# Performance work log

Measured on AMD Instinct MI355X. Metric: run time of the kernel, lower is better.

## Reference

```python
import jax, jax.numpy as jnp
import numpy as np

IN_F, OUT_F = 4096, 4096
IN_Q, OUT_Q = IN_F // 4, OUT_F // 4


def setup_inputs() -> dict:
    key = jax.random.key(0)
    kx, kr, ki, kj, kk = jax.random.split(key, 5)
    std = 1.0 / np.sqrt(IN_F)
    x = jax.random.normal(kx, (4, 2048, IN_F), dtype=jnp.float32)
    Wr = std * jax.random.normal(kr, (OUT_Q, IN_Q), dtype=jnp.float32)
    Wi = std * jax.random.normal(ki, (OUT_Q, IN_Q), dtype=jnp.float32)
    Wj = std * jax.random.normal(kj, (OUT_Q, IN_Q), dtype=jnp.float32)
    Wk = std * jax.random.normal(kk, (OUT_Q, IN_Q), dtype=jnp.float32)
    bias = jnp.zeros((OUT_F,), dtype=jnp.float32)
    return {"x": x, "Wr": Wr, "Wi": Wi, "Wj": Wj, "Wk": Wk, "bias": bias}


def _hamilton_block(Wr, Wi, Wj, Wk):
    # Assemble the structured [4*out_q, 4*in_q] Hamilton block weight so the
    # whole op is ONE large GEMM instead of 16 small ones (same math).
    row_r = jnp.concatenate([Wr, -Wi, -Wj, -Wk], axis=1)
    row_i = jnp.concatenate([Wi,  Wr,  Wk, -Wj], axis=1)
    row_j = jnp.concatenate([Wj, -Wk,  Wr,  Wi], axis=1)
    row_k = jnp.concatenate([Wk,  Wj, -Wi,  Wr], axis=1)
    return jnp.concatenate([row_r, row_i, row_j, row_k], axis=0)  # [OUT_F, IN_F]


def reference(x, Wr, Wi, Wj, Wk, bias):
    W = _hamilton_block(Wr, Wi, Wj, Wk)
    # x: [B, S, IN_F] @ W.T -> [B, S, OUT_F]
    out = jnp.einsum('bsf,of->bso', x, W) + bias
    return out
```

## Files before the change

kernel.cpp:

```cpp
#include <hip/hip_runtime.h>
#include <hip/hip_bf16.h>


#define M_DIM 8192
#define N_DIM 4096
#define K_DIM 4096
#define BK 64
#define NT (K_DIM / BK)

typedef __attribute__((ext_vector_type(8))) short bf16x8;
typedef __attribute__((ext_vector_type(4))) float f32x4;
typedef __attribute__((ext_vector_type(8))) unsigned short ushort8;

static __device__ __forceinline__ unsigned short f2bf(float f) {
    unsigned int u = __float_as_uint(f);
    return (unsigned short)((u + 0x7fffu + ((u >> 16) & 1u)) >> 16);
}
static __device__ __forceinline__ unsigned short f2bf_sgn(float f, unsigned int sg) {
    unsigned int u = __float_as_uint(f) ^ sg;
    return (unsigned short)((u + 0x7fffu + ((u >> 16) & 1u)) >> 16);
}

__global__ __launch_bounds__(256) void cvt_x_kernel(const float* __restrict__ x,
                                                    unsigned short* __restrict__ xb) {
    int i = (blockIdx.x * 256 + threadIdx.x) * 8;
    f32x4 a = __builtin_nontemporal_load((const f32x4*)(x + i));
    f32x4 b = __builtin_nontemporal_load((const f32x4*)(x + i + 4));
    ushort8 o;
    o[0] = f2bf(a[0]); o[1] = f2bf(a[1]); o[2] = f2bf(a[2]); o[3] = f2bf(a[3]);
    o[4] = f2bf(b[0]); o[5] = f2bf(b[1]); o[6] = f2bf(b[2]); o[7] = f2bf(b[3]);
    *(ushort8*)(xb + i) = o;
}

__global__ __launch_bounds__(256) void prep_w_kernel(const float* __restrict__ Wr,
    const float* __restrict__ Wi, const float* __restrict__ Wj,
    const float* __restrict__ Wk, unsigned short* __restrict__ wb) {
    int row = blockIdx.x >> 1;
    int col = ((blockIdx.x & 1) * 256 + threadIdx.x) * 8;
    int p = row >> 10, q = col >> 10;
    int ci = p ^ q;
    const float* src = (ci == 0) ? Wr : (ci == 1) ? Wi : (ci == 2) ? Wj : Wk;
    unsigned int sg = ((0x428Eu >> (p * 4 + q)) & 1u) << 31;
    int so = (row & 1023) * 1024 + (col & 1023);
    f32x4 a = *(const f32x4*)(src + so);
    f32x4 b = *(const f32x4*)(src + so + 4);
    ushort8 o;
    o[0] = f2bf_sgn(a[0], sg); o[1] = f2bf_sgn(a[1], sg);
    o[2] = f2bf_sgn(a[2], sg); o[3] = f2bf_sgn(a[3], sg);
    o[4] = f2bf_sgn(b[0], sg); o[5] = f2bf_sgn(b[1], sg);
    o[6] = f2bf_sgn(b[2], sg); o[7] = f2bf_sgn(b[3], sg);
    *(ushort8*)(wb + row * 4096 + col) = o;
}

#define GLD16(gp, lp) __builtin_amdgcn_global_load_lds( \
    (const __attribute__((address_space(1))) void*)(gp), \
    (__attribute__((address_space(3))) void*)(lp), 16, 0, 0)

#define BAR() do { asm volatile("" ::: "memory"); \
                   __builtin_amdgcn_s_barrier(); \
                   asm volatile("" ::: "memory"); } while (0)
#define VM(n) asm volatile("s_waitcnt vmcnt(" #n ")" ::: "memory")

static __device__ __forceinline__ f32x4 MF(bf16x8 a, bf16x8 b, f32x4 c) {
    return __builtin_amdgcn_mfma_f32_16x16x32_bf16(a, b, c, 0, 0, 0);
}

__global__ __launch_bounds__(512, 2) void qgemm_bf16(
    const unsigned short* __restrict__ A, const unsigned short* __restrict__ B,
    const float* __restrict__ bias, float* __restrict__ out)
{
    __shared__ __align__(16) unsigned short Lsh[2][2][2][128 * 64];

    int bid = blockIdx.x;
    int cpx = gridDim.x >> 3;
    int wg  = (bid & 7) * cpx + (bid >> 3);
    int brow = (wg >> 4) * 256;
    int bcol = (wg & 15) * 256;

    int tid   = threadIdx.x;
    int lane  = tid & 63;
    int wid   = tid >> 6;
    int hA    = wid >> 2;
    int nb    = wid & 3;
    int hB    = nb >> 1;
    int rB0   = (nb & 1) << 6;
    int fr    = lane & 15;
    int fslot = lane >> 4;

    const unsigned short* Ag = A + (size_t)brow * K_DIM;
    const unsigned short* Bg = B + (size_t)bcol * K_DIM;

    f32x4 acc[8][4] = {};

    auto stage = [&](int buf, int ab, int half, int t) {
        const unsigned short* g = (ab ? Bg : Ag) + (size_t)(half << 7) * K_DIM + t * BK;
        unsigned short* l = &Lsh[buf][ab][half][0];
        #pragma unroll
        for (int i = 0; i < 2; ++i) {
            int c = i * 512 + tid;
            int r = c >> 3, s = c & 7;
            GLD16(g + (size_t)r * K_DIM + ((s ^ (r & 7)) << 3), l + (c << 3));
        }
    };
    auto rdA = [&](int buf, int mi, int ks) -> bf16x8 {
        int r = mi * 16 + fr;
        int slot = (ks * 4 + fslot) ^ (r & 7);
        return *(const bf16x8*)((const char*)&Lsh[buf][0][hA][0] + r * 128 + (slot << 4));
    };
    auto rdB = [&](int buf, int ni, int ks) -> bf16x8 {
        int r = rB0 + ni * 16 + fr;
        int slot = (ks * 4 + fslot) ^ (r & 7);
        return *(const bf16x8*)((const char*)&Lsh[buf][1][hB][0] + r * 128 + (slot << 4));
    };

    stage(0, 0, 0, 0); stage(0, 0, 1, 0); stage(0, 1, 0, 0); stage(0, 1, 1, 0);
    stage(1, 1, 0, 1); stage(1, 1, 1, 1);
    VM(4); BAR();

    for (int t = 0; t < NT; ++t) {
        int buf = t & 1;
        bf16x8 bfrag[4][2];

        #pragma unroll
        for (int ni = 0; ni < 4; ++ni) {
            bfrag[ni][0] = rdB(buf, ni, 0);
            bfrag[ni][1] = rdB(buf, ni, 1);
        }
        {
            bf16x8 x0 = rdA(buf, 0, 0), x1 = rdA(buf, 0, 1);
            bf16x8 x2 = rdA(buf, 1, 0), x3 = rdA(buf, 1, 1);
            if (t + 1 < NT) { stage(buf ^ 1, 0, 0, t + 1); stage(buf ^ 1, 0, 1, t + 1); }
            BAR();
            __builtin_amdgcn_s_setprio(1);
            #pragma unroll
            for (int ni = 0; ni < 4; ++ni) {
                acc[0][ni] = MF(x0, bfrag[ni][0], acc[0][ni]);
                acc[0][ni] = MF(x1, bfrag[ni][1], acc[0][ni]);
                acc[1][ni] = MF(x2, bfrag[ni][0], acc[1][ni]);
                acc[1][ni] = MF(x3, bfrag[ni][1], acc[1][ni]);
            }
            __builtin_amdgcn_s_setprio(0);
            BAR();
        }
        {
            bf16x8 x0 = rdA(buf, 2, 0), x1 = rdA(buf, 2, 1);
            bf16x8 x2 = rdA(buf, 3, 0), x3 = rdA(buf, 3, 1);
            if (t + 2 < NT) stage(buf, 1, 0, t + 2);
            BAR();
            __builtin_amdgcn_s_setprio(1);
            #pragma unroll
            for (int ni = 0; ni < 4; ++ni) {
                acc[2][ni] = MF(x0, bfrag[ni][0], acc[2][ni]);
                acc[2][ni] = MF(x1, bfrag[ni][1], acc[2][ni]);
                acc[3][ni] = MF(x2, bfrag[ni][0], acc[3][ni]);
                acc[3][ni] = MF(x3, bfrag[ni][1], acc[3][ni]);
            }
            __builtin_amdgcn_s_setprio(0);
            BAR();
        }
        {
            bf16x8 x0 = rdA(buf, 4, 0), x1 = rdA(buf, 4, 1);
            bf16x8 x2 = rdA(buf, 5, 0), x3 = rdA(buf, 5, 1);
            if (t + 2 < NT) stage(buf, 1, 1, t + 2);
            BAR();
            __builtin_amdgcn_s_setprio(1);
            #pragma unroll
            for (int ni = 0; ni < 4; ++ni) {
                acc[4][ni] = MF(x0, bfrag[ni][0], acc[4][ni]);
                acc[4][ni] = MF(x1, bfrag[ni][1], acc[4][ni]);
                acc[5][ni] = MF(x2, bfrag[ni][0], acc[5][ni]);
                acc[5][ni] = MF(x3, bfrag[ni][1], acc[5][ni]);
            }
            __builtin_amdgcn_s_setprio(0);
            BAR();
        }
        {
            bf16x8 x0 = rdA(buf, 6, 0), x1 = rdA(buf, 6, 1);
            bf16x8 x2 = rdA(buf, 7, 0), x3 = rdA(buf, 7, 1);
            BAR();
            __builtin_amdgcn_s_setprio(1);
            #pragma unroll
            for (int ni = 0; ni < 4; ++ni) {
                acc[6][ni] = MF(x0, bfrag[ni][0], acc[6][ni]);
                acc[6][ni] = MF(x1, bfrag[ni][1], acc[6][ni]);
                acc[7][ni] = MF(x2, bfrag[ni][0], acc[7][ni]);
                acc[7][ni] = MF(x3, bfrag[ni][1], acc[7][ni]);
            }
            __builtin_amdgcn_s_setprio(0);
            if (t < NT - 2) { VM(4); } else { VM(0); }
            BAR();
        }
    }

    int cr = (lane >> 4) << 2;
    int cc = lane & 15;
    #pragma unroll
    for (int ni = 0; ni < 4; ++ni) {
        int col = bcol + nb * 64 + ni * 16 + cc;
        float bv = bias[col];
        #pragma unroll
        for (int mi = 0; mi < 8; ++mi) {
            int r0 = brow + hA * 128 + mi * 16 + cr;
            #pragma unroll
            for (int r = 0; r < 4; ++r)
                __builtin_nontemporal_store(acc[mi][ni][r] + bv,
                                            &out[(size_t)(r0 + r) * N_DIM + col]);
        }
    }
}

#define FBM 128
#define FBN 128
#define FBK 64
__global__ __launch_bounds__(256) void qgemm_fb(const float* __restrict__ x,
    const float* __restrict__ Wr, const float* __restrict__ Wi,
    const float* __restrict__ Wj, const float* __restrict__ Wk,
    const float* __restrict__ bias, float* __restrict__ out)
{
    __shared__ unsigned short As[FBM * FBK];
    __shared__ unsigned short Bs[FBN * FBK];

    int bid = blockIdx.x;
    int cpx = gridDim.x >> 3;
    int wg = (bid & 7) * cpx + (bid >> 3);
    int brow = (wg >> 5) * FBM;
    int bcol = (wg & 31) * FBN;

    int tid = threadIdx.x;
    int lane = tid & 63;
    int wv = tid >> 6;
    int wm = (wv >> 1) << 6;
    int wn = (wv & 1) << 6;
    int fr = lane & 15;
    int fk = (lane >> 4) << 3;

    int p = bcol >> 10;
    f32x4 acc[4][4] = {};

    for (int kt = 0; kt < K_DIM / FBK; ++kt) {
        int k0 = kt * FBK;
        int q = k0 >> 10;
        int ci = p ^ q;
        const float* wsrc = (ci == 0) ? Wr : (ci == 1) ? Wi : (ci == 2) ? Wj : Wk;
        unsigned int sg = ((0x428Eu >> (p * 4 + q)) & 1u) << 31;

        __syncthreads();
        #pragma unroll
        for (int i = 0; i < 4; ++i) {
            int c = i * 256 + tid;
            int row = c >> 3, colo = (c & 7) << 3;
            const float* s = x + (size_t)(brow + row) * K_DIM + k0 + colo;
            float4 a = *(const float4*)s;
            float4 b = *(const float4*)(s + 4);
            ushort8 o;
            o[0] = f2bf(a.x); o[1] = f2bf(a.y); o[2] = f2bf(a.z); o[3] = f2bf(a.w);
            o[4] = f2bf(b.x); o[5] = f2bf(b.y); o[6] = f2bf(b.z); o[7] = f2bf(b.w);
            *(ushort8*)(&As[c << 3]) = o;
        }
        #pragma unroll
        for (int i = 0; i < 4; ++i) {
            int c = i * 256 + tid;
            int row = c >> 3, colo = (c & 7) << 3;
            const float* s = wsrc + ((bcol + row) & 1023) * 1024 + ((k0 + colo) & 1023);
            float4 a = *(const float4*)s;
            float4 b = *(const float4*)(s + 4);
            ushort8 o;
            o[0] = f2bf_sgn(a.x, sg); o[1] = f2bf_sgn(a.y, sg);
            o[2] = f2bf_sgn(a.z, sg); o[3] = f2bf_sgn(a.w, sg);
            o[4] = f2bf_sgn(b.x, sg); o[5] = f2bf_sgn(b.y, sg);
            o[6] = f2bf_sgn(b.z, sg); o[7] = f2bf_sgn(b.w, sg);
            *(ushort8*)(&Bs[c << 3]) = o;
        }
        __syncthreads();

        #pragma unroll
        for (int ks = 0; ks < 2; ++ks) {
            bf16x8 af[4], bfr[4];
            #pragma unroll
            for (int m = 0; m < 4; ++m)
                af[m] = *(const bf16x8*)(&As[(wm + m * 16 + fr) * FBK + ks * 32 + fk]);
            #pragma unroll
            for (int n = 0; n < 4; ++n)
                bfr[n] = *(const bf16x8*)(&Bs[(wn + n * 16 + fr) * FBK + ks * 32 + fk]);
            #pragma unroll
            for (int m = 0; m < 4; ++m)
                #pragma unroll
                for (int n = 0; n < 4; ++n)
                    acc[m][n] = __builtin_amdgcn_mfma_f32_16x16x32_bf16(
                        af[m], bfr[n], acc[m][n], 0, 0, 0);
        }
    }

    int cr = (lane >> 4) << 2;
    int cc = lane & 15;
    #pragma unroll
    for (int n = 0; n < 4; ++n) {
        int col = bcol + wn + n * 16 + cc;
        float bv = bias[col];
        #pragma unroll
        for (int m = 0; m < 4; ++m) {
            int r0 = brow + wm + m * 16 + cr;
            #pragma unroll
            for (int r = 0; r < 4; ++r)
                out[(size_t)(r0 + r) * N_DIM + col] = acc[m][n][r] + bv;
        }
    }
}

extern "C" void kernel_launch(void* const* d_in, const int* in_sizes, int n_in,
                              void* d_out, int out_size, void* d_ws, size_t ws_size,
                              hipStream_t stream) {
    const float* x    = (const float*)d_in[0];
    const float* Wr   = (const float*)d_in[1];
    const float* Wi   = (const float*)d_in[2];
    const float* Wj   = (const float*)d_in[3];
    const float* Wk   = (const float*)d_in[4];
    const float* bias = (const float*)d_in[5];
    float* out = (float*)d_out;

    const size_t xb_bytes = (size_t)M_DIM * K_DIM * 2;
    const size_t wb_bytes = (size_t)N_DIM * K_DIM * 2;

    if (ws_size >= xb_bytes + wb_bytes) {
        unsigned short* xb = (unsigned short*)d_ws;
        unsigned short* wb = (unsigned short*)((char*)d_ws + xb_bytes);
        cvt_x_kernel<<<(M_DIM * K_DIM) / 2048, 256, 0, stream>>>(x, xb);
        prep_w_kernel<<<N_DIM * 2, 256, 0, stream>>>(Wr, Wi, Wj, Wk, wb);
        const int n_blocks = (M_DIM / 256) * (N_DIM / 256);
        qgemm_bf16<<<n_blocks, 512, 0, stream>>>(xb, wb, bias, out);
    } else {
        const int n_blocks = (M_DIM / FBM) * (N_DIM / FBN);
        qgemm_fb<<<n_blocks, 256, 0, stream>>>(x, Wr, Wi, Wj, Wk, bias, out);
    }
}
```

Before: 274.0 us.

## Cut per-iteration barriers from eight to two and interleave independent MFMA chains

The main K loop is restructured so each tile iteration uses two workgroup barriers instead of eight. The next tile's A stages are issued at the top of the iteration, and both B stages for t+2 are issued together after the first barrier, once every wave has read its B fragments into registers. The MFMAs in each sub-block are reordered so consecutive instructions update different accumulators, which avoids back-to-back dependencies on the same accumulator. The intent is to remove barrier stalls and keep the matrix pipe busier, at the cost of waves drifting further apart and more loads in flight at once.

```diff
diff --git a/kernel.cpp b/kernel.cpp
--- a/kernel.cpp
+++ b/kernel.cpp
@@ -113,14 +113,16 @@
         return *(const bf16x8*)((const char*)&Lsh[buf][1][hB][0] + r * 128 + (slot << 4));
     };
 
+    bf16x8 bfrag[4][2];
+
     stage(0, 0, 0, 0); stage(0, 0, 1, 0); stage(0, 1, 0, 0); stage(0, 1, 1, 0);
     stage(1, 1, 0, 1); stage(1, 1, 1, 1);
     VM(4); BAR();
 
     for (int t = 0; t < NT; ++t) {
         int buf = t & 1;
-        bf16x8 bfrag[4][2];
-
+
+        if (t + 1 < NT) { stage(buf ^ 1, 0, 0, t + 1); stage(buf ^ 1, 0, 1, t + 1); }
         #pragma unroll
         for (int ni = 0; ni < 4; ++ni) {
             bfrag[ni][0] = rdB(buf, ni, 0);
@@ -129,67 +131,64 @@
         {
             bf16x8 x0 = rdA(buf, 0, 0), x1 = rdA(buf, 0, 1);
             bf16x8 x2 = rdA(buf, 1, 0), x3 = rdA(buf, 1, 1);
-            if (t + 1 < NT) { stage(buf ^ 1, 0, 0, t + 1); stage(buf ^ 1, 0, 1, t + 1); }
-            BAR();
             __builtin_amdgcn_s_setprio(1);
             #pragma unroll
-            for (int ni = 0; ni < 4; ++ni) {
-                acc[0][ni] = MF(x0, bfrag[ni][0], acc[0][ni]);
-                acc[0][ni] = MF(x1, bfrag[ni][1], acc[0][ni]);
-                acc[1][ni] = MF(x2, bfrag[ni][0], acc[1][ni]);
-                acc[1][ni] = MF(x3, bfrag[ni][1], acc[1][ni]);
-            }
+            for (int ni = 0; ni < 4; ++ni) acc[0][ni] = MF(x0, bfrag[ni][0], acc[0][ni]);
+            #pragma unroll
+            for (int ni = 0; ni < 4; ++ni) acc[1][ni] = MF(x2, bfrag[ni][0], acc[1][ni]);
+            #pragma unroll
+            for (int ni = 0; ni < 4; ++ni) acc[0][ni] = MF(x1, bfrag[ni][1], acc[0][ni]);
+            #pragma unroll
+            for (int ni = 0; ni < 4; ++ni) acc[1][ni] = MF(x3, bfrag[ni][1], acc[1][ni]);
             __builtin_amdgcn_s_setprio(0);
-            BAR();
-        }
+        }
+        BAR();
+
+        if (t + 2 < NT) { stage(buf, 1, 0, t + 2); stage(buf, 1, 1, t + 2); }
         {
             bf16x8 x0 = rdA(buf, 2, 0), x1 = rdA(buf, 2, 1);
             bf16x8 x2 = rdA(buf, 3, 0), x3 = rdA(buf, 3, 1);
-            if (t + 2 < NT) stage(buf, 1, 0, t + 2);
-            BAR();
             __builtin_amdgcn_s_setprio(1);
             #pragma unroll
-            for (int ni = 0; ni < 4; ++ni) {
-                acc[2][ni] = MF(x0, bfrag[ni][0], acc[2][ni]);
-                acc[2][ni] = MF(x1, bfrag[ni][1], acc[2][ni]);
-                acc[3][ni] = MF(x2, bfrag[ni][0], acc[3][ni]);
-                acc[3][ni] = MF(x3, bfrag[ni][1], acc[3][ni]);
-            }
+            for (int ni = 0; ni < 4; ++ni) acc[2][ni] = MF(x0, bfrag[ni][0], acc[2][ni]);
+            #pragma unroll
+            for (int ni = 0; ni < 4; ++ni) acc[3][ni] = MF(x2, bfrag[ni][0], acc[3][ni]);
+            #pragma unroll
+            for (int ni = 0; ni < 4; ++ni) acc[2][ni] = MF(x1, bfrag[ni][1], acc[2][ni]);
+            #pragma unroll
+            for (int ni = 0; ni < 4; ++ni) acc[3][ni] = MF(x3, bfrag[ni][1], acc[3][ni]);
             __builtin_amdgcn_s_setprio(0);
-            BAR();
         }
         {
             bf16x8 x0 = rdA(buf, 4, 0), x1 = rdA(buf, 4, 1);
             bf16x8 x2 = rdA(buf, 5, 0), x3 = rdA(buf, 5, 1);
-            if (t + 2 < NT) stage(buf, 1, 1, t + 2);
-            BAR();
             __builtin_amdgcn_s_setprio(1);
             #pragma unroll
-            for (int ni = 0; ni < 4; ++ni) {
-                acc[4][ni] = MF(x0, bfrag[ni][0], acc[4][ni]);
-                acc[4][ni] = MF(x1, bfrag[ni][1], acc[4][ni]);
-                acc[5][ni] = MF(x2, bfrag[ni][0], acc[5][ni]);
-                acc[5][ni] = MF(x3, bfrag[ni][1], acc[5][ni]);
-            }
+            for (int ni = 0; ni < 4; ++ni) acc[4][ni] = MF(x0, bfrag[ni][0], acc[4][ni]);
+            #pragma unroll
+            for (int ni = 0; ni < 4; ++ni) acc[5][ni] = MF(x2, bfrag[ni][0], acc[5][ni]);
+            #pragma unroll
+            for (int ni = 0; ni < 4; ++ni) acc[4][ni] = MF(x1, bfrag[ni][1], acc[4][ni]);
+            #pragma unroll
+            for (int ni = 0; ni < 4; ++ni) acc[5][ni] = MF(x3, bfrag[ni][1], acc[5][ni]);
             __builtin_amdgcn_s_setprio(0);
-            BAR();
         }
         {
             bf16x8 x0 = rdA(buf, 6, 0), x1 = rdA(buf, 6, 1);
             bf16x8 x2 = rdA(buf, 7, 0), x3 = rdA(buf, 7, 1);
-            BAR();
             __builtin_amdgcn_s_setprio(1);
             #pragma unroll
-            for (int ni = 0; ni < 4; ++ni) {
-                acc[6][ni] = MF(x0, bfrag[ni][0], acc[6][ni]);
-                acc[6][ni] = MF(x1, bfrag[ni][1], acc[6][ni]);
-                acc[7][ni] = MF(x2, bfrag[ni][0], acc[7][ni]);
-                acc[7][ni] = MF(x3, bfrag[ni][1], acc[7][ni]);
-            }
+            for (int ni = 0; ni < 4; ++ni) acc[6][ni] = MF(x0, bfrag[ni][0], acc[6][ni]);
+            #pragma unroll
+            for (int ni = 0; ni < 4; ++ni) acc[7][ni] = MF(x2, bfrag[ni][0], acc[7][ni]);
+            #pragma unroll
+            for (int ni = 0; ni < 4; ++ni) acc[6][ni] = MF(x1, bfrag[ni][1], acc[6][ni]);
+            #pragma unroll
+            for (int ni = 0; ni < 4; ++ni) acc[7][ni] = MF(x3, bfrag[ni][1], acc[7][ni]);
             __builtin_amdgcn_s_setprio(0);
-            if (t < NT - 2) { VM(4); } else { VM(0); }
-            BAR();
-        }
+        }
+        if (t < NT - 2) { VM(4); } else { VM(0); }
+        BAR();
     }
 
     int cr = (lane >> 4) << 2;
```

Measured after the change: 273.8 us. About the same (-0.1%).
